# Kernel tuning notes

Hardware: AMD Instinct MI355X
Metric: run time of the kernel (lower is better)

The kernel has to match this reference:

```python
import jax, jax.numpy as jnp
import numpy as np
import math

B, S, D, H = 16, 256, 1024, 16
DK = D // H
MAXLEN = 512


def _sinusoid_table(maxlen, dim):
    # rows for positions -maxlen .. maxlen-1  (2*maxlen rows)
    pos = jnp.arange(-maxlen, maxlen, dtype=jnp.float32)[:, None]
    i = jnp.arange(dim)
    angle = pos / jnp.power(10000.0, (2 * (i // 2)) / dim).astype(jnp.float32)
    return jnp.where(i % 2 == 0, jnp.sin(angle), jnp.cos(angle))


def setup_inputs() -> dict:
    key = jax.random.key(0)
    ks = jax.random.split(key, 13)
    std_qk = math.sqrt(2.0 / (D + DK))
    inp = {
        "x": jax.random.normal(ks[0], (B, S, D), jnp.float32),
        "Wq": jax.random.normal(ks[1], (D, D), jnp.float32) * std_qk,
        "bq": jnp.zeros((D,), jnp.float32),
        "Wk": jax.random.normal(ks[2], (D, D), jnp.float32) * std_qk,
        "bk": jnp.zeros((D,), jnp.float32),
        "Wv": jax.random.normal(ks[3], (D, D), jnp.float32) * std_qk,
        "bv": jnp.zeros((D,), jnp.float32),
        "Wr": jax.random.normal(ks[4], (D, D), jnp.float32) * std_qk,
        "br": jnp.zeros((D,), jnp.float32),
        "u_bias": jax.random.normal(ks[5], (H, DK), jnp.float32) * math.sqrt(2.0 / (H + DK)),
        "v_bias": jax.random.normal(ks[6], (H, DK), jnp.float32) * math.sqrt(2.0 / (H + DK)),
        "Wo": jax.random.normal(ks[7], (D, D), jnp.float32) * math.sqrt(2.0 / (D + D)),
        "bo": jnp.zeros((D,), jnp.float32),
    }
    return inp


def reference(x, Wq, bq, Wk, bk, Wv, bv, Wr, br, u_bias, v_bias, Wo, bo):
    table = _sinusoid_table(MAXLEN, D)  # (2*MAXLEN, D)
    # relative position indices: idx[s, z] = z - s, shifted by +MAXLEN
    relpos_idx = (jnp.arange(2 * S)[None, :] - jnp.arange(S)[:, None])[:, :S] + MAXLEN
    relpos_vec = table[relpos_idx]  # (S, S, D)

    q = (x @ Wq.T + bq).reshape(B, S, H, DK)
    k = (x @ Wk.T + bk).reshape(B, S, H, DK)
    v = (x @ Wv.T + bv).reshape(B, S, H, DK)

    rp_k = (relpos_vec @ Wk.T + bk).reshape(S, S, H, DK)       # shared k_proj
    kR = (x @ Wr.T + br).reshape(B, S, H, DK)                  # relpos_k_proj(keys)
    rp_R = (relpos_vec @ Wr.T + br).reshape(S, S, H, DK)       # relpos_k_proj(relpos)

    w = jnp.einsum('bshd,bzhd->bhsz', q, k)
    w = w + jnp.einsum('bshd,szhd->bhsz', q, rp_k)
    w = w + jnp.einsum('hd,bzhd->bhz', u_bias, kR)[:, :, None, :]
    w = w + jnp.einsum('hd,szhd->hsz', v_bias, rp_R)[None, :, :, :]
    w = w / math.sqrt(DK)

    causal = jnp.tril(jnp.ones((S, S), jnp.float32))[None, None, :, :]
    w = w + jnp.log(causal)  # -inf above diagonal

    attn = jax.nn.softmax(w, axis=-1)                          # (B,H,S,S)
    vw = jnp.einsum('bhsz,bzhd->bshd', attn, v).reshape(B, S, D)
    return vw @ Wo.T + bo
```

## Files before the change

### kernel.cpp

```cpp
#include <hip/hip_runtime.h>
#include <math.h>

constexpr int kB  = 16;
constexpr int kS  = 256;
constexpr int kD  = 1024;
constexpr int kH  = 16;
constexpr float kScale = 0.125f;

using bf16x8  = __attribute__((ext_vector_type(8))) short;
using floatx4 = __attribute__((ext_vector_type(4))) float;
typedef unsigned short u16;

__device__ __forceinline__ u16 f2bf(float x) {
  union { float f; unsigned u; } v; v.f = x;
  unsigned r = v.u + 0x7fffu + ((v.u >> 16) & 1u);
  return (u16)(r >> 16);
}
__device__ __forceinline__ float bf2f(u16 h) {
  union { unsigned u; float f; } v; v.u = ((unsigned)h) << 16;
  return v.f;
}

#define MFMA16(a, b, c) __builtin_amdgcn_mfma_f32_16x16x32_bf16((a), (b), (c), 0, 0, 0)
#define GLL16(gp, lp)                                                        \
  __builtin_amdgcn_global_load_lds(                                          \
      (const __attribute__((address_space(1))) unsigned int*)(gp),           \
      (__attribute__((address_space(3))) unsigned int*)(lp), 16, 0, 0)

__global__ __launch_bounds__(256) void pack_k(
    const float* __restrict__ x, const float* __restrict__ Wq,
    const float* __restrict__ Wk, const float* __restrict__ Wv,
    const float* __restrict__ Wo,
    const float* __restrict__ bq, const float* __restrict__ bk,
    const float* __restrict__ bv,
    u16* __restrict__ xA, u16* __restrict__ W3b, u16* __restrict__ Wob,
    float* __restrict__ b3) {
  size_t i = ((size_t)blockIdx.x * 256 + threadIdx.x) * 4;
  const size_t NX = (size_t)4194304, NW = (size_t)1048576;
  const size_t BEND = NX + 4 * NW + 3072;
  const float* src;
  u16* dst;
  size_t o;
  if (i < NX) {
    src = x; dst = xA; o = i;
  } else if (i < NX + 3 * NW) {
    size_t j = i - NX;
    int sel = (int)(j >> 20);
    o = j & (NW - 1);
    src = sel == 0 ? Wq : sel == 1 ? Wv : Wk;
    dst = W3b + (size_t)sel * NW;
  } else if (i < NX + 4 * NW) {
    o = i - NX - 3 * NW;
    src = Wo; dst = Wob;
  } else if (i < BEND) {
    size_t j = i - NX - 4 * NW;
    int sel = (int)(j >> 10);
    o = j & 1023;
    src = sel == 0 ? bq : sel == 1 ? bv : bk;
    *reinterpret_cast<float4*>(b3 + j) = *reinterpret_cast<const float4*>(src + o);
    return;
  } else if (i < BEND + 262144) {
    size_t j = i - BEND;
    int p = (int)(j >> 10);
    int ibase = (int)(j & 1023);
    ushort4 r;
    u16* rr = (u16*)&r;
#pragma unroll
    for (int c = 0; c < 4; ++c) {
      int idx = ibase + c;
      float ex = (float)(2 * (idx / 2)) * (1.0f / 1024.0f);
      float scale = exp2f(ex * -13.287712379549449f);
      float angle = (float)(p - 255) * scale;
      rr[c] = f2bf((idx & 1) ? cosf(angle) : sinf(angle));
    }
    *reinterpret_cast<ushort4*>(xA + NX + j) = r;
    return;
  } else {
    return;
  }
  float4 v = *reinterpret_cast<const float4*>(src + o);
  ushort4 r;
  r.x = f2bf(v.x); r.y = f2bf(v.y); r.z = f2bf(v.z); r.w = f2bf(v.w);
  *reinterpret_cast<ushort4*>(dst + o) = r;
}

__global__ __launch_bounds__(256) void uv_fold_k(
    const float* __restrict__ Wr, const float* __restrict__ br,
    const float* __restrict__ ub, const float* __restrict__ vb,
    u16* __restrict__ W3b, float* __restrict__ b3) {
  int gid = blockIdx.x * 256 + threadIdx.x;
  int j = gid >> 10, c = gid & 1023;
  int h = j & 15;
  const float* bvec = (j < 16 ? ub : vb) + h * 64;
  const float* wcol = Wr + (size_t)(h * 64) * 1024 + c;
  float a = 0.f;
#pragma unroll
  for (int d = 0; d < 64; ++d) a += bvec[d] * wcol[(size_t)d * 1024];
  W3b[(size_t)(3072 + j) * 1024 + c] = f2bf(a);
  if (gid < 128) {
    float s = 0.f;
    if (gid < 32) {
      const float* bv2 = (gid < 16 ? ub : vb) + (gid & 15) * 64;
      const float* brp = br + (gid & 15) * 64;
      for (int d = 0; d < 64; ++d) s += bv2[d] * brp[d];
    }
    b3[3072 + gid] = s;
  }
}

template <int OUT_MODE>
__global__ __launch_bounds__(256) void gemm_k(
    const u16* __restrict__ A, const u16* __restrict__ W,
    const float* __restrict__ bias, void* __restrict__ Cv,
    int M, int N, int K, float* __restrict__ utb, float* __restrict__ dtb,
    int mTiles, int nTiles) {
  const int xcd = blockIdx.x & 7;
  const int li  = blockIdx.x >> 3;
  const int r0   = (xcd * mTiles) >> 3;
  const int rcnt = (((xcd + 1) * mTiles) >> 3) - r0;
  if (li >= rcnt * nTiles) return;
  const int bm = (r0 + li % rcnt) * 128;
  const int bn = (li / rcnt) * 128;

  __shared__ u16 Alds[128 * 64];
  __shared__ u16 Blds[128 * 64];
  const int t = threadIdx.x, w = t >> 6, l = t & 63;
  const int l15 = l & 15, quad = l >> 4;
  const int wm = w >> 1, wn = w & 1;
  const int lrow8 = l >> 3;
  const int kslot = l & 7;

  floatx4 acc[4][4] = {};

  for (int k0 = 0; k0 < K; k0 += 64) {
#pragma unroll
    for (int sg = 0; sg < 4; ++sg) {
      int mrow = sg * 32 + w * 8 + lrow8;
      int gk = (kslot ^ (mrow & 7)) << 3;
      GLL16(A + (size_t)(bm + mrow) * K + k0 + gk, Alds + (sg * 32 + w * 8) * 64);
      GLL16(W + (size_t)(bn + mrow) * K + k0 + gk, Blds + (sg * 32 + w * 8) * 64);
    }
    __syncthreads();
#pragma unroll
    for (int c = 0; c < 2; ++c) {
      bf16x8 af[4], bf[4];
#pragma unroll
      for (int mi = 0; mi < 4; ++mi) {
        int am = wm * 64 + mi * 16 + l15;
        af[mi] = *(const bf16x8*)(Alds + am * 64 + (((c * 4 + quad) ^ (am & 7)) << 3));
      }
#pragma unroll
      for (int ni = 0; ni < 4; ++ni) {
        int an = wn * 64 + ni * 16 + l15;
        bf[ni] = *(const bf16x8*)(Blds + an * 64 + (((c * 4 + quad) ^ (an & 7)) << 3));
      }
#pragma unroll
      for (int mi = 0; mi < 4; ++mi)
#pragma unroll
        for (int ni = 0; ni < 4; ++ni)
          acc[mi][ni] = MFMA16(af[mi], bf[ni], acc[mi][ni]);
    }
    __syncthreads();
  }

#pragma unroll
  for (int ni = 0; ni < 4; ++ni) {
    int col = bn + wn * 64 + ni * 16 + l15;
    float bv = bias[col];
#pragma unroll
    for (int mi = 0; mi < 4; ++mi) {
      int mrow = bm + wm * 64 + mi * 16 + quad * 4;
#pragma unroll
      for (int r = 0; r < 4; ++r) {
        float v = acc[mi][ni][r] + bv;
        int row = mrow + r;
        if (OUT_MODE == 0) {
          ((float*)Cv)[(size_t)row * N + col] = v;
        } else {
          if (col < 3072) {
            int matsel = col >> 10;
            int hh = (col >> 6) & 15, dd = col & 63;
            if (row < 4096) {
              int bb = row >> 8, ss = row & 255;
              ((u16*)Cv)[(size_t)matsel * 4194304 +
                         ((size_t)(((bb << 4) + hh) << 8) + ss) * 64 + dd] = f2bf(v);
            } else if (matsel == 2) {
              int pp = row - 4096;
              ((u16*)Cv)[(size_t)3 * 4194304 +
                         ((size_t)((hh << 8) + pp)) * 64 + dd] = f2bf(v);
            }
          } else if (col < 3088) {
            if (row < 4096)
              utb[((row >> 8) * 16 + (col - 3072)) * 256 + (row & 255)] = v;
          } else if (col < 3104) {
            if (row >= 4096)
              dtb[(col - 3088) * 256 + (row - 4096)] = v;
          }
        }
      }
    }
  }
}

__global__ __launch_bounds__(512, 2) void attn_k(
    const u16* __restrict__ Qh, const u16* __restrict__ Kh,
    const u16* __restrict__ Vh, const u16* __restrict__ RPKh,
    const float* __restrict__ ut, const float* __restrict__ dt,
    u16* __restrict__ vw) {
  __shared__ u16 Klds[256 * 64];
  __shared__ u16 Vt[64][280];
  __shared__ float Sc[32][257];
  __shared__ float Sc2[32][257];
  __shared__ float Ut[256], Dt[256], Rinv[32];

  const int bh = blockIdx.x;
  const int h = bh & 15;
  const int b = bh >> 4;
  const size_t bh256 = (size_t)bh << 8;

  const int t = threadIdx.x, w = t >> 6, l = t & 63;
  const int l15 = l & 15, quad = l >> 4;

  {
    const int lrow8 = l >> 3, kslot = l & 7;
#pragma unroll
    for (int i = 0; i < 4; ++i) {
      int row = w * 32 + i * 8 + lrow8;
      int gk = (kslot ^ (row & 7)) << 3;
      GLL16(Kh + (bh256 + row) * 64 + gk, Klds + (w * 32 + i * 8) * 64);
    }
  }
  {
    int z = t & 255, dh = t >> 8;
    const u16* gp = Vh + (bh256 + z) * 64 + dh * 32;
    ushort4 vv[8];
#pragma unroll
    for (int i = 0; i < 8; ++i) vv[i] = *(const ushort4*)(gp + i * 4);
#pragma unroll
    for (int i = 0; i < 8; ++i) {
      Vt[dh * 32 + i * 4 + 0][z] = vv[i].x;
      Vt[dh * 32 + i * 4 + 1][z] = vv[i].y;
      Vt[dh * 32 + i * 4 + 2][z] = vv[i].z;
      Vt[dh * 32 + i * 4 + 3][z] = vv[i].w;
    }
  }
  if (t < 256) Ut[t] = ut[bh256 + t];
  else         Dt[t - 256] = dt[((size_t)h << 8) + (t - 256)];
  __syncthreads();

  for (int st = 0; st < 8; ++st) {
    const int s0 = st * 32;

    bf16x8 qa[2][2];
#pragma unroll
    for (int rt = 0; rt < 2; ++rt) {
      const u16* qp = Qh + (bh256 + s0 + rt * 16 + l15) * 64 + quad * 8;
      qa[rt][0] = *(const bf16x8*)qp;
      qa[rt][1] = *(const bf16x8*)(qp + 32);
    }

    {
      int cnt = 0;
#pragma unroll
      for (int rt = 0; rt < 2; ++rt) {
        const int rB = s0 + rt * 16;
        const int nzt = 2 * st + rt + 1;
        for (int zt = 0; zt < nzt; ++zt, ++cnt) {
          if ((cnt & 7) != w) continue;
          const int zr = (zt << 4) + l15;
          const u16* krow = Klds + zr * 64;
          bf16x8 kb0 = *(const bf16x8*)(krow + ((quad ^ (zr & 7)) << 3));
          bf16x8 kb1 = *(const bf16x8*)(krow + (((quad + 4) ^ (zr & 7)) << 3));
          floatx4 acc = {};
          acc = MFMA16(qa[rt][0], kb0, acc);
          acc = MFMA16(qa[rt][1], kb1, acc);
          float u = Ut[zr];
#pragma unroll
          for (int r = 0; r < 4; ++r)
            Sc[rt * 16 + quad * 4 + r][zr] = acc[r] + u;
        }
        for (int j = 0; j < nzt; ++j, ++cnt) {
          if ((cnt & 7) != w) continue;
          const int pr = 240 - rB + (j << 4) + l15;
          const u16* rp = RPKh + ((size_t)(h << 8) + pr) * 64 + quad * 8;
          bf16x8 rb0 = *(const bf16x8*)rp;
          bf16x8 rb1 = *(const bf16x8*)(rp + 32);
          floatx4 acc = {};
          acc = MFMA16(qa[rt][0], rb0, acc);
          acc = MFMA16(qa[rt][1], rb1, acc);
          float dv = Dt[pr];
#pragma unroll
          for (int r = 0; r < 4; ++r)
            Sc2[rt * 16 + quad * 4 + r][pr] = acc[r] + dv;
        }
      }
    }
    __syncthreads();

    {
      const int row = w * 4 + (l >> 4);
      const int c16 = l & 15;
      const int s = s0 + row;
      const int zfill = 32 * (st + 1);
      float m = -1e30f;
      for (int z = c16; z <= s; z += 16)
        m = fmaxf(m, Sc[row][z] + Sc2[row][z - s + 255]);
      m = fmaxf(m, __shfl_xor(m, 1));
      m = fmaxf(m, __shfl_xor(m, 2));
      m = fmaxf(m, __shfl_xor(m, 4));
      m = fmaxf(m, __shfl_xor(m, 8));
      m *= kScale;
      float sum = 0.f;
      for (int z = c16; z < zfill; z += 16) {
        float e = 0.f;
        if (z <= s) {
          e = __expf((Sc[row][z] + Sc2[row][z - s + 255]) * kScale - m);
          sum += e;
        }
        Sc[row][z] = e;
      }
      sum += __shfl_xor(sum, 1);
      sum += __shfl_xor(sum, 2);
      sum += __shfl_xor(sum, 4);
      sum += __shfl_xor(sum, 8);
      if (c16 == 0) Rinv[row] = 1.f / sum;
    }
    __syncthreads();

    {
      const int strip = w >> 2, nt = w & 3;
      const int sB = s0 + strip * 16;
      floatx4 oacc = {};
      for (int kc = 0; kc <= st; ++kc) {
        const float* prow = &Sc[strip * 16 + l15][kc * 32 + quad * 8];
        bf16x8 pa;
        pa[0] = (short)f2bf(prow[0]); pa[1] = (short)f2bf(prow[1]);
        pa[2] = (short)f2bf(prow[2]); pa[3] = (short)f2bf(prow[3]);
        pa[4] = (short)f2bf(prow[4]); pa[5] = (short)f2bf(prow[5]);
        pa[6] = (short)f2bf(prow[6]); pa[7] = (short)f2bf(prow[7]);
        const u16* vp = &Vt[nt * 16 + l15][kc * 32 + quad * 8];
        bf16x8 vbf = *(const bf16x8*)vp;
        oacc = MFMA16(pa, vbf, oacc);
      }
#pragma unroll
      for (int r = 0; r < 4; ++r) {
        float ivr = Rinv[strip * 16 + quad * 4 + r];
        int srow = sB + quad * 4 + r;
        vw[(size_t)(b * 256 + srow) * 1024 + h * 64 + nt * 16 + l15] =
            f2bf(oacc[r] * ivr);
      }
    }
    __syncthreads();
  }
}

extern "C" void kernel_launch(void* const* d_in, const int* in_sizes, int n_in,
                              void* d_out, int out_size, void* d_ws, size_t ws_size,
                              hipStream_t stream) {
  const float* x  = (const float*)d_in[0];
  const float* Wq = (const float*)d_in[1];
  const float* bq = (const float*)d_in[2];
  const float* Wk = (const float*)d_in[3];
  const float* bk = (const float*)d_in[4];
  const float* Wv = (const float*)d_in[5];
  const float* bv = (const float*)d_in[6];
  const float* Wr = (const float*)d_in[7];
  const float* br = (const float*)d_in[8];
  const float* ub = (const float*)d_in[9];
  const float* vb = (const float*)d_in[10];
  const float* Wo = (const float*)d_in[11];
  const float* bo = (const float*)d_in[12];
  float* out = (float*)d_out;

  char* base = (char*)d_ws;
  size_t off = 0;
  auto alloc = [&](size_t bytes) {
    void* p = base + off;
    off += (bytes + 255) & ~(size_t)255;
    return p;
  };

  const size_t MAT = (size_t)4194304;
  u16*   xA    = (u16*)alloc((size_t)4352 * 1024 * 2);
  u16*   W3b   = (u16*)alloc((size_t)3200 * 1024 * 2);
  u16*   Wob   = (u16*)alloc((size_t)1024 * 1024 * 2);
  float* b3    = (float*)alloc((size_t)3200 * 4);
  u16*   Ph    = (u16*)alloc((3 * MAT + 262144) * 2);
  float* utb   = (float*)alloc((size_t)65536 * 4);
  float* dtb   = (float*)alloc((size_t)4096 * 4);
  u16*   vwb   = (u16*)alloc((size_t)4096 * 1024 * 2);

  u16* Qh   = Ph;
  u16* Vh   = Ph + MAT;
  u16* Kh   = Ph + 2 * MAT;
  u16* RPKh = Ph + 3 * MAT;

  pack_k<<<dim3(8451), dim3(256), 0, stream>>>(x, Wq, Wk, Wv, Wo, bq, bk, bv,
                                               xA, W3b, Wob, b3);
  uv_fold_k<<<dim3(128), dim3(256), 0, stream>>>(Wr, br, ub, vb, W3b, b3);

  gemm_k<2><<<dim3(1000), dim3(256), 0, stream>>>(xA, W3b, b3, Ph,
                                                  4352, 3200, 1024, utb, dtb, 34, 25);

  attn_k<<<dim3(256), dim3(512), 0, stream>>>(Qh, Kh, Vh, RPKh, utb, dtb, vwb);

  gemm_k<0><<<dim3(256), dim3(256), 0, stream>>>(vwb, Wob, bo, out,
                                                 4096, 1024, 1024, nullptr, nullptr,
                                                 32, 8);
}
```

Before: 230.0 us.

## Use 256x256-tile phased MFMA GEMM for fused QKV/relpos projection

Adds a new GEMM kernel with 256x256 output tiles, 8 waves per block and double-buffered LDS with XOR swizzling. It interleaves global-to-LDS staging of the next k-tile with four MFMA phases under raised wave priority. Blocks are assigned XCD-aware across row tiles. The projection weights are padded to 3328 rows to fit whole tiles. The aim is more data reuse per loaded byte and better overlap of loads with MFMA, at the cost of only 221 tiles, which may leave CUs idle and lengthen the tail.

```diff
diff --git a/kernel.cpp b/kernel.cpp
--- a/kernel.cpp
+++ b/kernel.cpp
@@ -176,26 +176,150 @@
         int row = mrow + r;
         if (OUT_MODE == 0) {
           ((float*)Cv)[(size_t)row * N + col] = v;
-        } else {
-          if (col < 3072) {
-            int matsel = col >> 10;
-            int hh = (col >> 6) & 15, dd = col & 63;
-            if (row < 4096) {
-              int bb = row >> 8, ss = row & 255;
-              ((u16*)Cv)[(size_t)matsel * 4194304 +
-                         ((size_t)(((bb << 4) + hh) << 8) + ss) * 64 + dd] = f2bf(v);
-            } else if (matsel == 2) {
-              int pp = row - 4096;
-              ((u16*)Cv)[(size_t)3 * 4194304 +
-                         ((size_t)((hh << 8) + pp)) * 64 + dd] = f2bf(v);
-            }
-          } else if (col < 3088) {
-            if (row < 4096)
-              utb[((row >> 8) * 16 + (col - 3072)) * 256 + (row & 255)] = v;
-          } else if (col < 3104) {
-            if (row >= 4096)
-              dtb[(col - 3088) * 256 + (row - 4096)] = v;
+        }
+      }
+    }
+  }
+}
+
+#define PHASE_MFMA(aa, bb, mh, nh)                                             \
+  do {                                                                         \
+    __builtin_amdgcn_s_barrier();                                              \
+    asm volatile("s_waitcnt lgkmcnt(0)" ::: "memory");                         \
+    __builtin_amdgcn_sched_barrier(0);                                         \
+    __builtin_amdgcn_s_setprio(1);                                             \
+    _Pragma("unroll") for (int kc = 0; kc < 2; ++kc)                           \
+        _Pragma("unroll") for (int i = 0; i < 4; ++i)                          \
+            _Pragma("unroll") for (int j = 0; j < 2; ++j)                      \
+                acc[(mh) * 4 + i][(nh) * 2 + j] = MFMA16(                      \
+                    aa[kc][i], bb[kc][j], acc[(mh) * 4 + i][(nh) * 2 + j]);    \
+    __builtin_amdgcn_s_setprio(0);                                             \
+  } while (0)
+
+__global__ __launch_bounds__(512, 2) void gemm256_k(
+    const u16* __restrict__ A, const u16* __restrict__ W,
+    const float* __restrict__ bias, u16* __restrict__ Cv,
+    int K, float* __restrict__ utb, float* __restrict__ dtb,
+    int mTiles, int nTiles) {
+  const int xcd = blockIdx.x & 7;
+  const int li  = blockIdx.x >> 3;
+  const int r0   = (xcd * mTiles) >> 3;
+  const int rcnt = (((xcd + 1) * mTiles) >> 3) - r0;
+  if (li >= rcnt * nTiles) return;
+  const int bm = (r0 + li % rcnt) * 256;
+  const int bn = (li / rcnt) * 256;
+
+  __shared__ u16 lds[2 * 32768];
+
+  const int t = threadIdx.x, w = t >> 6, l = t & 63;
+  const int l15 = l & 15, quad = l >> 4;
+  const int wm = w >> 2, wn = w & 3;
+
+  const int NT = K >> 6;
+  floatx4 acc[8][4] = {};
+
+  auto stage = [&](int kt, int h) {
+    const u16* srcm = (h < 2) ? A : W;
+    const int baser = ((h < 2) ? bm : bn) + (h & 1) * 128;
+    u16* dst = lds + (kt & 1) * 32768 + h * 8192 + w * 512;
+    const int k0 = kt << 6;
+#pragma unroll
+    for (int j = 0; j < 2; ++j) {
+      int sub = w * 8 + (l >> 3) + j * 64;
+      int gk = ((l & 7) ^ (sub & 7)) << 3;
+      GLL16(srcm + (size_t)(baser + sub) * K + k0 + gk, dst + j * 4096);
+    }
+  };
+
+  stage(0, 0); stage(0, 1); stage(0, 2); stage(0, 3);
+  stage(1, 0);
+  asm volatile("s_waitcnt vmcnt(2)" ::: "memory");
+  __builtin_amdgcn_s_barrier();
+
+  for (int kt = 0; kt < NT; ++kt) {
+    const u16* LA = lds + (kt & 1) * 32768;
+    const u16* LB = LA + 16384;
+    bf16x8 a0[2][4], a1[2][4], b0[2][2], b1[2][2];
+
+#pragma unroll
+    for (int i = 0; i < 4; ++i) {
+      int am = wm * 128 + i * 16 + l15;
+      const u16* p = LA + am * 64;
+      a0[0][i] = *(const bf16x8*)(p + ((quad ^ (am & 7)) << 3));
+      a0[1][i] = *(const bf16x8*)(p + (((4 + quad) ^ (am & 7)) << 3));
+    }
+#pragma unroll
+    for (int j = 0; j < 2; ++j) {
+      int an = wn * 64 + j * 16 + l15;
+      const u16* p = LB + an * 64;
+      b0[0][j] = *(const bf16x8*)(p + ((quad ^ (an & 7)) << 3));
+      b0[1][j] = *(const bf16x8*)(p + (((4 + quad) ^ (an & 7)) << 3));
+    }
+    if (kt + 1 < NT) stage(kt + 1, 1);
+    PHASE_MFMA(a0, b0, 0, 0);
+    __builtin_amdgcn_s_barrier();
+
+#pragma unroll
+    for (int j = 0; j < 2; ++j) {
+      int an = wn * 64 + (2 + j) * 16 + l15;
+      const u16* p = LB + an * 64;
+      b1[0][j] = *(const bf16x8*)(p + ((quad ^ (an & 7)) << 3));
+      b1[1][j] = *(const bf16x8*)(p + (((4 + quad) ^ (an & 7)) << 3));
+    }
+    if (kt + 1 < NT) stage(kt + 1, 2);
+    PHASE_MFMA(a0, b1, 0, 1);
+    __builtin_amdgcn_s_barrier();
+
+#pragma unroll
+    for (int i = 0; i < 4; ++i) {
+      int am = wm * 128 + (4 + i) * 16 + l15;
+      const u16* p = LA + am * 64;
+      a1[0][i] = *(const bf16x8*)(p + ((quad ^ (am & 7)) << 3));
+      a1[1][i] = *(const bf16x8*)(p + (((4 + quad) ^ (am & 7)) << 3));
+    }
+    if (kt + 1 < NT) stage(kt + 1, 3);
+    PHASE_MFMA(a1, b0, 1, 0);
+    __builtin_amdgcn_s_barrier();
+
+    if (kt + 2 < NT) stage(kt + 2, 0);
+    PHASE_MFMA(a1, b1, 1, 1);
+    if (kt + 2 < NT) {
+      asm volatile("s_waitcnt vmcnt(2)" ::: "memory");
+    } else {
+      asm volatile("s_waitcnt vmcnt(0)" ::: "memory");
+    }
+    __builtin_amdgcn_s_barrier();
+  }
+
+#pragma unroll
+  for (int ni = 0; ni < 4; ++ni) {
+    int col = bn + wn * 64 + ni * 16 + l15;
+    float bv = bias[col];
+#pragma unroll
+    for (int mi = 0; mi < 8; ++mi) {
+      int mrow = bm + wm * 128 + mi * 16 + quad * 4;
+#pragma unroll
+      for (int r = 0; r < 4; ++r) {
+        float v = acc[mi][ni][r] + bv;
+        int row = mrow + r;
+        if (col < 3072) {
+          int matsel = col >> 10;
+          int hh = (col >> 6) & 15, dd = col & 63;
+          if (row < 4096) {
+            int bb = row >> 8, ss = row & 255;
+            Cv[(size_t)matsel * 4194304 +
+               ((size_t)(((bb << 4) + hh) << 8) + ss) * 64 + dd] = f2bf(v);
+          } else if (matsel == 2) {
+            int pp = row - 4096;
+            Cv[(size_t)3 * 4194304 +
+               ((size_t)((hh << 8) + pp)) * 64 + dd] = f2bf(v);
           }
+        } else if (col < 3088) {
+          if (row < 4096)
+            utb[((row >> 8) * 16 + (col - 3072)) * 256 + (row & 255)] = v;
+        } else if (col < 3104) {
+          if (row >= 4096)
+            dtb[(col - 3088) * 256 + (row - 4096)] = v;
         }
       }
     }
@@ -382,9 +506,9 @@
 
   const size_t MAT = (size_t)4194304;
   u16*   xA    = (u16*)alloc((size_t)4352 * 1024 * 2);
-  u16*   W3b   = (u16*)alloc((size_t)3200 * 1024 * 2);
+  u16*   W3b   = (u16*)alloc((size_t)3328 * 1024 * 2);
   u16*   Wob   = (u16*)alloc((size_t)1024 * 1024 * 2);
-  float* b3    = (float*)alloc((size_t)3200 * 4);
+  float* b3    = (float*)alloc((size_t)3328 * 4);
   u16*   Ph    = (u16*)alloc((3 * MAT + 262144) * 2);
   float* utb   = (float*)alloc((size_t)65536 * 4);
   float* dtb   = (float*)alloc((size_t)4096 * 4);
@@ -399,8 +523,8 @@
                                                xA, W3b, Wob, b3);
   uv_fold_k<<<dim3(128), dim3(256), 0, stream>>>(Wr, br, ub, vb, W3b, b3);
 
-  gemm_k<2><<<dim3(1000), dim3(256), 0, stream>>>(xA, W3b, b3, Ph,
-                                                  4352, 3200, 1024, utb, dtb, 34, 25);
+  gemm256_k<<<dim3(312), dim3(512), 0, stream>>>(xA, W3b, b3, Ph,
+                                                 1024, utb, dtb, 17, 13);
 
   attn_k<<<dim3(256), dim3(512), 0, stream>>>(Qh, Kh, Vh, RPKh, utb, dtb, vwb);
 
```

Measured after the change: 266.4 us. 15.8% more time.
